# Optimization experiments

Hardware: AMD Instinct MI355X
Metric: run time of the kernel (lower is better)

Reference implementation:

```python
import jax, jax.numpy as jnp
import numpy as np

B, T, D, H = 2, 2048, 1024, 16
HD = D // H  # 64
EPS = 1e-5

def _ln(x, g, b):
    mu = jnp.mean(x, axis=-1, keepdims=True)
    var = jnp.mean(jnp.square(x - mu), axis=-1, keepdims=True)
    return (x - mu) * jax.lax.rsqrt(var + EPS) * g + b

def setup_inputs() -> dict:
    key = jax.random.key(0)
    ks = jax.random.split(key, 12)
    s = 0.02
    return {
        "x":  jax.random.normal(ks[0], (B, T, D), jnp.float32),
        "Wq": jax.random.normal(ks[1], (H, D, HD), jnp.float32) * s,
        "Wk": jax.random.normal(ks[2], (H, D, HD), jnp.float32) * s,
        "Wv": jax.random.normal(ks[3], (H, D, HD), jnp.float32) * s,
        "Wo": jax.random.normal(ks[4], (D, D), jnp.float32) * s,
        "bo": jnp.zeros((D,), jnp.float32),
        "W1": jax.random.normal(ks[5], (D, 4 * D), jnp.float32) * s,
        "b1": jnp.zeros((4 * D,), jnp.float32),
        "W2": jax.random.normal(ks[6], (4 * D, D), jnp.float32) * s,
        "b2": jnp.zeros((D,), jnp.float32),
        "ln1_g": jnp.ones((D,), jnp.float32),
        "ln1_b": jnp.zeros((D,), jnp.float32),
        "ln2_g": jnp.ones((D,), jnp.float32),
        "ln2_b": jnp.zeros((D,), jnp.float32),
    }

def reference(x, Wq, Wk, Wv, Wo, bo, W1, b1, W2, b2, ln1_g, ln1_b, ln2_g, ln2_b):
    b, t, d = x.shape
    # --- self-attention on ln1(x) ---
    h = _ln(x, ln1_g, ln1_b)
    q = jnp.einsum('btd,hde->bhte', h, Wq)  # [B,H,T,hd]
    k = jnp.einsum('btd,hde->bhte', h, Wk)
    v = jnp.einsum('btd,hde->bhte', h, Wv)
    # NOTE: original code scales by C**-0.5 with C = N_EMBED (not head_size)
    wei = jnp.einsum('bhte,bhse->bhts', q, k) * (d ** -0.5)
    causal = jnp.tril(jnp.ones((t, t), bool))
    wei = jnp.where(causal, wei, -jnp.inf)
    att = jax.nn.softmax(wei, axis=-1)
    o = jnp.einsum('bhts,bhse->bhte', att, v)
    o = o.transpose(0, 2, 1, 3).reshape(b, t, d)  # concat heads
    x = x + o @ Wo + bo
    # --- feed-forward on ln2(x) ---
    h2 = _ln(x, ln2_g, ln2_b)
    ff = jax.nn.relu(h2 @ W1 + b1) @ W2 + b2
    return x + ff
```

## Files before the change

### kernel.cpp

```cpp
#include <hip/hip_runtime.h>
#include <stdint.h>

typedef unsigned short u16;
typedef __attribute__((ext_vector_type(8))) short bf16x8;
typedef __attribute__((ext_vector_type(4))) float f32x4;
typedef __attribute__((ext_vector_type(4))) unsigned int u32x4;
typedef __attribute__((ext_vector_type(2))) unsigned int u32x2;
typedef __attribute__((ext_vector_type(4))) unsigned short u16x4;

#define MFMA16(a, b, c) __builtin_amdgcn_mfma_f32_16x16x32_bf16(a, b, c, 0, 0, 0)
#define VMCNT(N) asm volatile("s_waitcnt vmcnt(" #N ")" ::: "memory")
#define LGKM0() asm volatile("s_waitcnt lgkmcnt(0)" ::: "memory")

__device__ __forceinline__ u16 f2bf(float f) {
  union { float f; uint32_t u; } v; v.f = f;
  uint32_t r = v.u + 0x7FFFu + ((v.u >> 16) & 1u);
  return (u16)(r >> 16);
}

__device__ __forceinline__ float bf2f(u16 u) {
  union { uint32_t u; float f; } v; v.u = ((uint32_t)u) << 16;
  return v.f;
}

__device__ __forceinline__ uint32_t cvt_pk_bf16(float a, float b) {
  uint32_t r;
  asm("v_cvt_pk_bf16_f32 %0, %1, %2" : "=v"(r) : "v"(a), "v"(b));
  return r;
}

__device__ __forceinline__ void gload_lds16(const u16* g, u16* l) {
  __builtin_amdgcn_global_load_lds((const __attribute__((address_space(1))) void*)(g),
                                   (__attribute__((address_space(3))) void*)(l), 16, 0, 0);
}

__global__ __launch_bounds__(256) void prep_kernel(
    const float* __restrict__ x, const float* __restrict__ g1,
    const float* __restrict__ be1, u16* __restrict__ h,
    const float* __restrict__ Wq, const float* __restrict__ Wk,
    const float* __restrict__ Wv, u16* __restrict__ BtQKV,
    const float* __restrict__ Wo, u16* __restrict__ WoT,
    const float* __restrict__ W1, u16* __restrict__ W1T,
    const float* __restrict__ W2, u16* __restrict__ W2T) {
  __shared__ float tile[32][33];
  __shared__ float red[8];
  int bid = blockIdx.x, tid = threadIdx.x;
  if (bid < 4096) {
    int row = bid;
    float4 v = ((const float4*)(x + (size_t)row * 1024))[tid];
    float s = v.x + v.y + v.z + v.w;
    float ss = v.x * v.x + v.y * v.y + v.z * v.z + v.w * v.w;
#pragma unroll
    for (int m = 1; m < 64; m <<= 1) { s += __shfl_xor(s, m); ss += __shfl_xor(ss, m); }
    int wave = tid >> 6, lane = tid & 63;
    if (lane == 0) { red[wave] = s; red[4 + wave] = ss; }
    __syncthreads();
    s = red[0] + red[1] + red[2] + red[3];
    ss = red[4] + red[5] + red[6] + red[7];
    float mean = s * (1.0f / 1024.0f);
    float var = ss * (1.0f / 1024.0f) - mean * mean;
    float rstd = rsqrtf(var + 1e-5f);
    float4 gv = ((const float4*)g1)[tid];
    float4 bv = ((const float4*)be1)[tid];
    u16x4 o;
    o.x = f2bf((v.x - mean) * rstd * gv.x + bv.x);
    o.y = f2bf((v.y - mean) * rstd * gv.y + bv.y);
    o.z = f2bf((v.z - mean) * rstd * gv.z + bv.z);
    o.w = f2bf((v.w - mean) * rstd * gv.w + bv.w);
    *(u16x4*)(h + (size_t)row * 1024 + tid * 4) = o;
    return;
  }
  const float* I;
  u16* O;
  int K, N, n0, k0;
  if (bid < 7168) {
    int idx = bid - 4096;
    int bz = idx >> 6, by = (idx >> 1) & 31, bx = idx & 1;
    int ww = bz >> 4, head = bz & 15;
    I = ((ww == 0) ? Wq : (ww == 1) ? Wk : Wv) + (size_t)head * 65536;
    O = BtQKV + (size_t)ww * 1048576 + (size_t)head * 65536;
    K = 1024; N = 64; n0 = bx * 32; k0 = by * 32;
  } else if (bid < 8192) {
    int idx = bid - 7168;
    I = Wo; O = WoT; K = 1024; N = 1024;
    n0 = (idx & 31) * 32; k0 = (idx >> 5) * 32;
  } else if (bid < 12288) {
    int idx = bid - 8192;
    I = W1; O = W1T; K = 1024; N = 4096;
    n0 = (idx & 127) * 32; k0 = (idx >> 7) * 32;
  } else {
    int idx = bid - 12288;
    I = W2; O = W2T; K = 4096; N = 1024;
    n0 = (idx & 31) * 32; k0 = (idx >> 5) * 32;
  }
  int tx = tid & 31, ty = tid >> 5;
#pragma unroll
  for (int i = 0; i < 4; i++)
    tile[ty + i * 8][tx] = I[(size_t)(k0 + ty + i * 8) * N + n0 + tx];
  __syncthreads();
#pragma unroll
  for (int i = 0; i < 4; i++)
    O[(size_t)(n0 + ty + i * 8) * K + k0 + tx] = f2bf(tile[tx][ty + i * 8]);
}

__global__ __launch_bounds__(256) void combine_ln(const float* __restrict__ x,
                                                  const u16* __restrict__ p,
                                                  const float* __restrict__ bo,
                                                  const float* __restrict__ g,
                                                  const float* __restrict__ beta,
                                                  float* __restrict__ out,
                                                  u16* __restrict__ h2) {
  int row = blockIdx.x;
  int tid = threadIdx.x;
  size_t i = (size_t)row * 1024 + tid * 4;
  float4 v = *(const float4*)(x + i);
  float4 bb = *(const float4*)(bo + tid * 4);
  v.x += bb.x; v.y += bb.y; v.z += bb.z; v.w += bb.w;
#pragma unroll
  for (int z = 0; z < 4; z++) {
    u16x4 pv = *(const u16x4*)(p + (size_t)z * 4096 * 1024 + i);
    v.x += bf2f(pv.x); v.y += bf2f(pv.y); v.z += bf2f(pv.z); v.w += bf2f(pv.w);
  }
  *(float4*)(out + i) = v;
  float s = v.x + v.y + v.z + v.w;
  float ss = v.x * v.x + v.y * v.y + v.z * v.z + v.w * v.w;
#pragma unroll
  for (int m = 1; m < 64; m <<= 1) { s += __shfl_xor(s, m); ss += __shfl_xor(ss, m); }
  __shared__ float red[8];
  int wave = tid >> 6, lane = tid & 63;
  if (lane == 0) { red[wave] = s; red[4 + wave] = ss; }
  __syncthreads();
  s = red[0] + red[1] + red[2] + red[3];
  ss = red[4] + red[5] + red[6] + red[7];
  float mean = s * (1.0f / 1024.0f);
  float var = ss * (1.0f / 1024.0f) - mean * mean;
  float rstd = rsqrtf(var + 1e-5f);
  float4 gv = ((const float4*)g)[tid];
  float4 bv = ((const float4*)beta)[tid];
  u16x4 o;
  o.x = f2bf((v.x - mean) * rstd * gv.x + bv.x);
  o.y = f2bf((v.y - mean) * rstd * gv.y + bv.y);
  o.z = f2bf((v.z - mean) * rstd * gv.z + bv.z);
  o.w = f2bf((v.w - mean) * rstd * gv.w + bv.w);
  *(u16x4*)(h2 + i) = o;
}

template <int EP>
__global__ __launch_bounds__(512, 2) void gemm8p(const u16* __restrict__ A,
                                                 const u16* __restrict__ Bt,
                                                 int M, int N, int K, int KS,
                                                 void* __restrict__ out0,
                                                 u16* __restrict__ out1,
                                                 u16* __restrict__ out2,
                                                 const float* __restrict__ bias) {
  __shared__ __align__(16) u16 lds[65536];
  const int tid = threadIdx.x;
  const int lane = tid & 63, wave = tid >> 6;
  const int lo = lane & 15, hi = lane >> 4;
  const int wm = wave >> 2, wn = wave & 3;
  int gx = gridDim.x;
  int lin = blockIdx.y * gx + blockIdx.x;
  int nwg = gx * gridDim.y;
  int cpx = nwg >> 3;
  int swz = (lin & 7) * cpx + (lin >> 3);
  int bm0 = (swz / gx) * 256, bn0 = (swz % gx) * 256;
  int kbeg = blockIdx.z * KS;
  int T = KS >> 6;

  int rs_ = tid >> 3, ss_ = (tid & 7) ^ (rs_ & 7);
  const u16* srcA = A + (size_t)(bm0 + rs_) * K + kbeg + ss_ * 8;
  const u16* srcB = Bt + (size_t)(bn0 + rs_) * K + kbeg + ss_ * 8;
  const size_t i1 = (size_t)64 * K;
  const size_t h1 = (size_t)128 * K;
  const int dst0 = wave * 512;
  const int dst1 = 4096 + wave * 512;

  const int rpA = wm * 16 + lo;
  const int rpB = wn * 16 + lo;
  const int sp0 = (hi ^ (lo & 7)) * 8;

  f32x4 acc[8][4] = {};
  bf16x8 a[4][2], b0[2][2], b1[2][2];

  auto stageA = [&](int buf, int h, int koff) {
    const u16* s = srcA + koff + (h ? h1 : 0);
    u16* d = lds + (buf * 2 + h) * 8192;
    gload_lds16(s, d + dst0);
    gload_lds16(s + i1, d + dst1);
  };
  auto stageB = [&](int buf, int h, int koff) {
    const u16* s = srcB + koff + (h ? h1 : 0);
    u16* d = lds + 32768 + (buf * 2 + h) * 8192;
    gload_lds16(s, d + dst0);
    gload_lds16(s + i1, d + dst1);
  };
  auto loadA = [&](int buf, int h) {
    const u16* base = lds + (buf * 2 + h) * 8192 + rpA * 64;
#pragma unroll
    for (int m = 0; m < 4; m++) {
      a[m][0] = *(const bf16x8*)(base + m * 2048 + sp0);
      a[m][1] = *(const bf16x8*)(base + m * 2048 + (sp0 ^ 32));
    }
  };
  auto loadB = [&](bf16x8 (&bb)[2][2], int buf, int g) {
    const u16* base = lds + 32768 + (buf * 2 + g) * 8192 + rpB * 64;
#pragma unroll
    for (int n = 0; n < 2; n++) {
      bb[n][0] = *(const bf16x8*)(base + n * 4096 + sp0);
      bb[n][1] = *(const bf16x8*)(base + n * 4096 + (sp0 ^ 32));
    }
  };
  auto mmac = [&](int mh, int np, bf16x8 (&bb)[2][2]) {
    __builtin_amdgcn_s_setprio(1);
#pragma unroll
    for (int m = 0; m < 4; m++)
#pragma unroll
      for (int n = 0; n < 2; n++) {
        acc[mh + m][np + n] = MFMA16(a[m][0], bb[n][0], acc[mh + m][np + n]);
        acc[mh + m][np + n] = MFMA16(a[m][1], bb[n][1], acc[mh + m][np + n]);
      }
    __builtin_amdgcn_s_setprio(0);
  };

  stageA(0, 0, 0); stageB(0, 0, 0); stageB(0, 1, 0); stageA(0, 1, 0);
  VMCNT(4);
  __builtin_amdgcn_s_barrier();

  for (int t = 0; t < T; ++t) {
    int cur = t & 1, nxt = cur ^ 1;
    bool more = (t + 1 < T);
    int koff = (t + 1) * 64;
    loadA(cur, 0); loadB(b0, cur, 0);
    if (more) stageA(nxt, 0, koff);
    __builtin_amdgcn_s_barrier();
    LGKM0();
    __builtin_amdgcn_sched_barrier(0);
    mmac(0, 0, b0);
    __builtin_amdgcn_s_barrier();
    loadB(b1, cur, 1);
    if (more) { stageB(nxt, 0, koff); VMCNT(6); } else { VMCNT(2); }
    __builtin_amdgcn_s_barrier();
    LGKM0();
    __builtin_amdgcn_sched_barrier(0);
    mmac(0, 2, b1);
    __builtin_amdgcn_s_barrier();
    loadA(cur, 1);
    if (more) { stageB(nxt, 1, koff); VMCNT(6); } else { VMCNT(0); }
    __builtin_amdgcn_s_barrier();
    LGKM0();
    __builtin_amdgcn_sched_barrier(0);
    mmac(4, 0, b0);
    __builtin_amdgcn_s_barrier();
    if (more) { stageA(nxt, 1, koff); VMCNT(4); }
    __builtin_amdgcn_s_barrier();
    mmac(4, 2, b1);
    __builtin_amdgcn_s_barrier();
  }

  const int sec = (EP == 0) ? (bn0 >> 10) : 0;
#pragma unroll
  for (int mt = 0; mt < 8; mt++) {
    int gr0 = bm0 + (mt >> 2) * 128 + (mt & 3) * 32 + wm * 16 + hi * 4;
#pragma unroll
    for (int nt = 0; nt < 4; nt++) {
      int gc = bn0 + (nt >> 1) * 128 + (nt & 1) * 64 + wn * 16 + lo;
      if constexpr (EP == 0) {
        int b_ = gr0 >> 11, t_ = gr0 & 2047;
        int nn = gc & 1023, h_ = nn >> 6, e_ = nn & 63;
        size_t bh = (size_t)(b_ * 16 + h_);
        if (sec == 2) {
          u32x2 w;
          w.x = cvt_pk_bf16(acc[mt][nt][0], acc[mt][nt][1]);
          w.y = cvt_pk_bf16(acc[mt][nt][2], acc[mt][nt][3]);
          *(u32x2*)(out2 + (bh * 64 + e_) * 2048 + t_) = w;
        } else {
          float sc = (sec == 0) ? 0.0450842200f : 1.0f;
          u16* dst = (sec == 0) ? (u16*)out0 : out1;
#pragma unroll
          for (int j = 0; j < 4; j++)
            dst[(bh * 2048 + t_ + j) * 64 + e_] = f2bf(acc[mt][nt][j] * sc);
        }
      } else {
#pragma unroll
        for (int j = 0; j < 4; j++) {
          int gr = gr0 + j;
          float val = acc[mt][nt][j];
          if constexpr (EP == 2) {
            float v = val + bias[gc];
            ((u16*)out0)[(size_t)gr * N + gc] = f2bf(fmaxf(v, 0.0f));
          } else if constexpr (EP == 4) {
            ((u16*)out0)[(size_t)blockIdx.z * M * N + (size_t)gr * N + gc] = f2bf(val);
          }
        }
      }
    }
  }
}

__global__ __launch_bounds__(256) void combine4(float* __restrict__ out,
                                                const float* __restrict__ res,
                                                const u16* __restrict__ p,
                                                const float* __restrict__ bias) {
  size_t i = ((size_t)blockIdx.x * 256 + threadIdx.x) * 4;
  float4 r = *(const float4*)(res + i);
  float4 bb = *(const float4*)(bias + (i & 1023));
  float a0 = r.x + bb.x, a1 = r.y + bb.y, a2 = r.z + bb.z, a3 = r.w + bb.w;
#pragma unroll
  for (int z = 0; z < 4; z++) {
    u16x4 v = *(const u16x4*)(p + (size_t)z * 4096 * 1024 + i);
    a0 += bf2f(v.x); a1 += bf2f(v.y); a2 += bf2f(v.z); a3 += bf2f(v.w);
  }
  float4 o4 = {a0, a1, a2, a3};
  *(float4*)(out + i) = o4;
}

__global__ __launch_bounds__(512, 4) void attn_kernel(const u16* __restrict__ q,
                                                      const u16* __restrict__ k,
                                                      const u16* __restrict__ vt,
                                                      u16* __restrict__ o) {
  __shared__ __align__(16) u16 Ks[2][64 * 64];
  __shared__ __align__(16) u16 Vs[2][64 * 64];
  __shared__ __align__(16) u16 Ps[8][16 * 72];
  int bh = blockIdx.y;
  int pi = blockIdx.x;
  int tid = threadIdx.x, lane = tid & 63, wave = tid >> 6;
  int lo = lane & 15, hi = lane >> 4;
  int grp = wave >> 2;
  int qblk_w = grp ? pi : (31 - pi);
  int qb0 = qblk_w * 64;
  int nkb = 32 - pi;
  const u16* qbase = q + (size_t)bh * 2048 * 64;
  const u16* kbase = k + (size_t)bh * 2048 * 64;
  const u16* vbase = vt + (size_t)bh * 64 * 2048;

  int srow = tid >> 3;
  int ssl = (tid & 7) ^ (srow & 7);
  int kOff = srow * 64 + ssl * 8;
  int vOff = srow * 2048 + ssl * 8;

  int qrow = qb0 + (wave & 3) * 16 + lo;
  bf16x8 qf0 = *(const bf16x8*)(qbase + (size_t)qrow * 64 + hi * 8);
  bf16x8 qf1 = *(const bf16x8*)(qbase + (size_t)qrow * 64 + 32 + hi * 8);

  float l_r = 0.0f;
  f32x4 of[4] = {};
  u16* Pw = Ps[wave];

  auto stage = [&](int b, int kb) {
    gload_lds16(kbase + (size_t)kb * 4096 + kOff, Ks[b] + wave * 512);
    gload_lds16(vbase + kb * 64 + vOff, Vs[b] + wave * 512);
  };

  stage(0, 0);
  __syncthreads();

  for (int kb = 0; kb < nkb; kb++) {
    int cur = kb & 1;
    if (kb + 1 < nkb) stage(cur ^ 1, kb + 1);
    if (kb <= qblk_w) {
      const u16* Kb = Ks[cur];
      const u16* Vb = Vs[cur];
      f32x4 s4[4] = {};
#pragma unroll
      for (int nt = 0; nt < 4; nt++) {
        int r = nt * 16 + lo, rw = r & 7;
        bf16x8 kf0 = *(const bf16x8*)(Kb + r * 64 + ((hi ^ rw) << 3));
        bf16x8 kf1 = *(const bf16x8*)(Kb + r * 64 + (((hi + 4) ^ rw) << 3));
        s4[nt] = MFMA16(kf0, qf0, s4[nt]);
        s4[nt] = MFMA16(kf1, qf1, s4[nt]);
      }
      float rs = 0.0f;
      bool diag = (kb == qblk_w);
#pragma unroll
      for (int nt = 0; nt < 4; nt++) {
        float e0, e1, e2, e3;
        if (diag) {
          int key = kb * 64 + nt * 16 + hi * 4;
          e0 = (key     > qrow) ? 0.0f : __builtin_amdgcn_exp2f(s4[nt][0]);
          e1 = (key + 1 > qrow) ? 0.0f : __builtin_amdgcn_exp2f(s4[nt][1]);
          e2 = (key + 2 > qrow) ? 0.0f : __builtin_amdgcn_exp2f(s4[nt][2]);
          e3 = (key + 3 > qrow) ? 0.0f : __builtin_amdgcn_exp2f(s4[nt][3]);
        } else {
          e0 = __builtin_amdgcn_exp2f(s4[nt][0]);
          e1 = __builtin_amdgcn_exp2f(s4[nt][1]);
          e2 = __builtin_amdgcn_exp2f(s4[nt][2]);
          e3 = __builtin_amdgcn_exp2f(s4[nt][3]);
        }
        rs += (e0 + e1) + (e2 + e3);
        u32x2 w;
        w.x = cvt_pk_bf16(e0, e1);
        w.y = cvt_pk_bf16(e2, e3);
        *(u32x2*)(Pw + lo * 72 + nt * 16 + hi * 4) = w;
      }
      rs += __shfl_xor(rs, 16);
      rs += __shfl_xor(rs, 32);
      l_r += rs;
      bf16x8 pb0 = *(const bf16x8*)(Pw + lo * 72 + hi * 8);
      bf16x8 pb1 = *(const bf16x8*)(Pw + lo * 72 + 32 + hi * 8);
#pragma unroll
      for (int et = 0; et < 4; et++) {
        int e = et * 16 + lo, ew = e & 7;
        bf16x8 v0 = *(const bf16x8*)(Vb + e * 64 + ((hi ^ ew) << 3));
        bf16x8 v1 = *(const bf16x8*)(Vb + e * 64 + (((hi + 4) ^ ew) << 3));
        of[et] = MFMA16(v0, pb0, of[et]);
        of[et] = MFMA16(v1, pb1, of[et]);
      }
    }
    __syncthreads();
  }
  int hh = bh & 15, bb = bh >> 4;
  float inv = 1.0f / l_r;
  size_t obase = ((size_t)(bb * 2048 + qrow)) * 1024 + hh * 64 + hi * 4;
#pragma unroll
  for (int et = 0; et < 4; et++) {
    u32x2 w;
    w.x = cvt_pk_bf16(of[et][0] * inv, of[et][1] * inv);
    w.y = cvt_pk_bf16(of[et][2] * inv, of[et][3] * inv);
    *(u32x2*)(o + obase + et * 16) = w;
  }
}

extern "C" void kernel_launch(void* const* d_in, const int* in_sizes, int n_in,
                              void* d_out, int out_size, void* d_ws, size_t ws_size,
                              hipStream_t stream) {
  const float* x = (const float*)d_in[0];
  const float* Wq = (const float*)d_in[1];
  const float* Wk = (const float*)d_in[2];
  const float* Wv = (const float*)d_in[3];
  const float* Wo = (const float*)d_in[4];
  const float* bo = (const float*)d_in[5];
  const float* W1 = (const float*)d_in[6];
  const float* b1 = (const float*)d_in[7];
  const float* W2 = (const float*)d_in[8];
  const float* b2 = (const float*)d_in[9];
  const float* g1 = (const float*)d_in[10];
  const float* be1 = (const float*)d_in[11];
  const float* g2 = (const float*)d_in[12];
  const float* be2 = (const float*)d_in[13];
  float* out = (float*)d_out;
  char* ws = (char*)d_ws;
  const size_t MB = 1024ull * 1024ull;

  u16* h = (u16*)(ws + 0);
  u16* o = h;
  u16* BtQKV = (u16*)(ws + 8 * MB);
  u16* WoT = (u16*)(ws + 14 * MB);
  u16* W1T = (u16*)(ws + 16 * MB);
  u16* W2T = (u16*)(ws + 64 * MB);
  u16* qb = (u16*)(ws + 32 * MB);
  u16* kb = (u16*)(ws + 40 * MB);
  u16* vtb = (u16*)(ws + 48 * MB);
  u16* h2 = (u16*)(ws + 8 * MB);
  u16* pwo = (u16*)(ws + 32 * MB);
  u16* yb = (u16*)(ws + 32 * MB);
  u16* pf2 = (u16*)(ws + 0);

  prep_kernel<<<16384, 256, 0, stream>>>(x, g1, be1, h, Wq, Wk, Wv, BtQKV,
                                         Wo, WoT, W1, W1T, W2, W2T);
  gemm8p<0><<<dim3(12, 16), 512, 0, stream>>>(h, BtQKV, 4096, 3072, 1024, 1024,
                                              (void*)qb, kb, vtb, nullptr);
  attn_kernel<<<dim3(16, 32), 512, 0, stream>>>(qb, kb, vtb, o);
  gemm8p<4><<<dim3(4, 16, 4), 512, 0, stream>>>(o, WoT, 4096, 1024, 1024, 256,
                                                (void*)pwo, nullptr, nullptr, nullptr);
  combine_ln<<<4096, 256, 0, stream>>>(x, pwo, bo, g2, be2, out, h2);
  gemm8p<2><<<dim3(16, 16), 512, 0, stream>>>(h2, W1T, 4096, 4096, 1024, 1024,
                                              (void*)yb, nullptr, nullptr, b1);
  gemm8p<4><<<dim3(4, 16, 4), 512, 0, stream>>>(yb, W2T, 4096, 1024, 4096, 1024,
                                                (void*)pf2, nullptr, nullptr, nullptr);
  combine4<<<4096, 256, 0, stream>>>(out, out, pf2, b2);
}
```

Before: 209.5 us.

## Replace split-K output GEMMs with 128x128 tile GEMM fusing bias and residual

The Wo and W2 projections were split-K GEMMs that wrote four bf16 partial outputs, followed by separate combine kernels. They are replaced by a new 128x128-tile GEMM with 256 threads that covers the full K range and adds bias and residual directly in its epilogue, writing fp32. The LN2 kernel now only normalizes. This removes the partial-sum memory traffic and two reduction passes. In exchange there is less parallelism per GEMM (256 workgroups, no K split), and partial sums are no longer rounded to bf16.

```diff
diff --git a/kernel.cpp b/kernel.cpp
--- a/kernel.cpp
+++ b/kernel.cpp
@@ -103,25 +103,13 @@
     O[(size_t)(n0 + ty + i * 8) * K + k0 + tx] = f2bf(tile[tx][ty + i * 8]);
 }
 
-__global__ __launch_bounds__(256) void combine_ln(const float* __restrict__ x,
-                                                  const u16* __restrict__ p,
-                                                  const float* __restrict__ bo,
-                                                  const float* __restrict__ g,
-                                                  const float* __restrict__ beta,
-                                                  float* __restrict__ out,
-                                                  u16* __restrict__ h2) {
+__global__ __launch_bounds__(256) void ln_kernel(const float* __restrict__ x,
+                                                 const float* __restrict__ g,
+                                                 const float* __restrict__ beta,
+                                                 u16* __restrict__ out) {
   int row = blockIdx.x;
   int tid = threadIdx.x;
-  size_t i = (size_t)row * 1024 + tid * 4;
-  float4 v = *(const float4*)(x + i);
-  float4 bb = *(const float4*)(bo + tid * 4);
-  v.x += bb.x; v.y += bb.y; v.z += bb.z; v.w += bb.w;
-#pragma unroll
-  for (int z = 0; z < 4; z++) {
-    u16x4 pv = *(const u16x4*)(p + (size_t)z * 4096 * 1024 + i);
-    v.x += bf2f(pv.x); v.y += bf2f(pv.y); v.z += bf2f(pv.z); v.w += bf2f(pv.w);
-  }
-  *(float4*)(out + i) = v;
+  float4 v = ((const float4*)(x + (size_t)row * 1024))[tid];
   float s = v.x + v.y + v.z + v.w;
   float ss = v.x * v.x + v.y * v.y + v.z * v.z + v.w * v.w;
 #pragma unroll
@@ -142,7 +130,7 @@
   o.y = f2bf((v.y - mean) * rstd * gv.y + bv.y);
   o.z = f2bf((v.z - mean) * rstd * gv.z + bv.z);
   o.w = f2bf((v.w - mean) * rstd * gv.w + bv.w);
-  *(u16x4*)(h2 + i) = o;
+  *(u16x4*)(out + (size_t)row * 1024 + tid * 4) = o;
 }
 
 template <int EP>
@@ -280,38 +268,141 @@
           for (int j = 0; j < 4; j++)
             dst[(bh * 2048 + t_ + j) * 64 + e_] = f2bf(acc[mt][nt][j] * sc);
         }
-      } else {
+      } else if constexpr (EP == 2) {
 #pragma unroll
         for (int j = 0; j < 4; j++) {
           int gr = gr0 + j;
-          float val = acc[mt][nt][j];
-          if constexpr (EP == 2) {
-            float v = val + bias[gc];
-            ((u16*)out0)[(size_t)gr * N + gc] = f2bf(fmaxf(v, 0.0f));
-          } else if constexpr (EP == 4) {
-            ((u16*)out0)[(size_t)blockIdx.z * M * N + (size_t)gr * N + gc] = f2bf(val);
-          }
+          float v = acc[mt][nt][j] + bias[gc];
+          ((u16*)out0)[(size_t)gr * N + gc] = f2bf(fmaxf(v, 0.0f));
         }
       }
     }
   }
 }
 
-__global__ __launch_bounds__(256) void combine4(float* __restrict__ out,
-                                                const float* __restrict__ res,
-                                                const u16* __restrict__ p,
-                                                const float* __restrict__ bias) {
-  size_t i = ((size_t)blockIdx.x * 256 + threadIdx.x) * 4;
-  float4 r = *(const float4*)(res + i);
-  float4 bb = *(const float4*)(bias + (i & 1023));
-  float a0 = r.x + bb.x, a1 = r.y + bb.y, a2 = r.z + bb.z, a3 = r.w + bb.w;
-#pragma unroll
-  for (int z = 0; z < 4; z++) {
-    u16x4 v = *(const u16x4*)(p + (size_t)z * 4096 * 1024 + i);
-    a0 += bf2f(v.x); a1 += bf2f(v.y); a2 += bf2f(v.z); a3 += bf2f(v.w);
-  }
-  float4 o4 = {a0, a1, a2, a3};
-  *(float4*)(out + i) = o4;
+__global__ __launch_bounds__(256, 2) void gemm128(const u16* __restrict__ A,
+                                                  const u16* __restrict__ Bt,
+                                                  int M, int N, int K,
+                                                  const float* __restrict__ bias,
+                                                  const float* __restrict__ res,
+                                                  float* __restrict__ out) {
+  __shared__ __align__(16) u16 lds[32768];
+  const int tid = threadIdx.x;
+  const int lane = tid & 63, wave = tid >> 6;
+  const int lo = lane & 15, hi = lane >> 4;
+  const int wm = wave >> 1, wn = wave & 1;
+  int gx = gridDim.x;
+  int lin = blockIdx.y * gx + blockIdx.x;
+  int nwg = gx * gridDim.y;
+  int cpx = nwg >> 3;
+  int swz = (lin & 7) * cpx + (lin >> 3);
+  int bm0 = (swz / gx) * 128, bn0 = (swz % gx) * 128;
+  int T = K >> 6;
+
+  int rs_ = tid >> 3, ss_ = (tid & 7) ^ (rs_ & 7);
+  const u16* srcA = A + (size_t)(bm0 + rs_) * K + ss_ * 8;
+  const u16* srcB = Bt + (size_t)(bn0 + rs_) * K + ss_ * 8;
+  const size_t i1 = (size_t)32 * K;
+  const size_t h1 = (size_t)64 * K;
+  const int dst0 = wave * 512;
+  const int dst1 = 2048 + wave * 512;
+
+  const int sp0 = (hi ^ (lo & 7)) * 8;
+
+  f32x4 acc[4][4] = {};
+  bf16x8 a[4][2], b[4][2];
+
+  auto stageA = [&](int buf, int h, int koff) {
+    const u16* s = srcA + koff + (h ? h1 : 0);
+    u16* d = lds + (buf * 2 + h) * 4096;
+    gload_lds16(s, d + dst0);
+    gload_lds16(s + i1, d + dst1);
+  };
+  auto stageB = [&](int buf, int h, int koff) {
+    const u16* s = srcB + koff + (h ? h1 : 0);
+    u16* d = lds + 16384 + (buf * 2 + h) * 4096;
+    gload_lds16(s, d + dst0);
+    gload_lds16(s + i1, d + dst1);
+  };
+  auto loadAh = [&](int buf, int h) {
+    const u16* base = lds + (buf * 2 + h) * 4096;
+#pragma unroll
+    for (int m = 0; m < 2; m++) {
+      int lr = m * 32 + wm * 16 + lo;
+      a[h * 2 + m][0] = *(const bf16x8*)(base + lr * 64 + sp0);
+      a[h * 2 + m][1] = *(const bf16x8*)(base + lr * 64 + (sp0 ^ 32));
+    }
+  };
+  auto loadBh = [&](int buf, int h) {
+    const u16* base = lds + 16384 + (buf * 2 + h) * 4096;
+#pragma unroll
+    for (int n = 0; n < 2; n++) {
+      int lr = n * 32 + wn * 16 + lo;
+      b[h * 2 + n][0] = *(const bf16x8*)(base + lr * 64 + sp0);
+      b[h * 2 + n][1] = *(const bf16x8*)(base + lr * 64 + (sp0 ^ 32));
+    }
+  };
+  auto mmac = [&](int mb, int nb) {
+    __builtin_amdgcn_s_setprio(1);
+#pragma unroll
+    for (int m = 0; m < 2; m++)
+#pragma unroll
+      for (int n = 0; n < 2; n++) {
+        acc[mb + m][nb + n] = MFMA16(a[mb + m][0], b[nb + n][0], acc[mb + m][nb + n]);
+        acc[mb + m][nb + n] = MFMA16(a[mb + m][1], b[nb + n][1], acc[mb + m][nb + n]);
+      }
+    __builtin_amdgcn_s_setprio(0);
+  };
+
+  stageA(0, 0, 0); stageB(0, 0, 0); stageB(0, 1, 0); stageA(0, 1, 0);
+  VMCNT(4);
+  __builtin_amdgcn_s_barrier();
+
+  for (int t = 0; t < T; ++t) {
+    int cur = t & 1, nxt = cur ^ 1;
+    bool more = (t + 1 < T);
+    int koff = (t + 1) * 64;
+    loadAh(cur, 0); loadBh(cur, 0);
+    if (more) { stageA(nxt, 0, koff); VMCNT(4); } else { VMCNT(2); }
+    __builtin_amdgcn_s_barrier();
+    LGKM0();
+    __builtin_amdgcn_sched_barrier(0);
+    mmac(0, 0);
+    __builtin_amdgcn_s_barrier();
+    loadBh(cur, 1);
+    if (more) { stageB(nxt, 0, koff); VMCNT(4); } else { VMCNT(0); }
+    __builtin_amdgcn_s_barrier();
+    LGKM0();
+    __builtin_amdgcn_sched_barrier(0);
+    mmac(0, 2);
+    __builtin_amdgcn_s_barrier();
+    loadAh(cur, 1);
+    if (more) stageB(nxt, 1, koff);
+    __builtin_amdgcn_s_barrier();
+    LGKM0();
+    __builtin_amdgcn_sched_barrier(0);
+    mmac(2, 0);
+    __builtin_amdgcn_s_barrier();
+    if (more) { stageA(nxt, 1, koff); VMCNT(4); }
+    __builtin_amdgcn_s_barrier();
+    mmac(2, 2);
+    __builtin_amdgcn_s_barrier();
+  }
+
+#pragma unroll
+  for (int mt = 0; mt < 4; mt++) {
+    int gr0 = bm0 + mt * 32 + wm * 16 + hi * 4;
+#pragma unroll
+    for (int nt = 0; nt < 4; nt++) {
+      int gc = bn0 + nt * 32 + wn * 16 + lo;
+      float bb = bias[gc];
+#pragma unroll
+      for (int j = 0; j < 4; j++) {
+        int gr = gr0 + j;
+        out[(size_t)gr * N + gc] = acc[mt][nt][j] + bb + res[(size_t)gr * N + gc];
+      }
+    }
+  }
 }
 
 __global__ __launch_bounds__(512, 4) void attn_kernel(const u16* __restrict__ q,
@@ -451,21 +542,16 @@
   u16* kb = (u16*)(ws + 40 * MB);
   u16* vtb = (u16*)(ws + 48 * MB);
   u16* h2 = (u16*)(ws + 8 * MB);
-  u16* pwo = (u16*)(ws + 32 * MB);
   u16* yb = (u16*)(ws + 32 * MB);
-  u16* pf2 = (u16*)(ws + 0);
 
   prep_kernel<<<16384, 256, 0, stream>>>(x, g1, be1, h, Wq, Wk, Wv, BtQKV,
                                          Wo, WoT, W1, W1T, W2, W2T);
   gemm8p<0><<<dim3(12, 16), 512, 0, stream>>>(h, BtQKV, 4096, 3072, 1024, 1024,
                                               (void*)qb, kb, vtb, nullptr);
   attn_kernel<<<dim3(16, 32), 512, 0, stream>>>(qb, kb, vtb, o);
-  gemm8p<4><<<dim3(4, 16, 4), 512, 0, stream>>>(o, WoT, 4096, 1024, 1024, 256,
-                                                (void*)pwo, nullptr, nullptr, nullptr);
-  combine_ln<<<4096, 256, 0, stream>>>(x, pwo, bo, g2, be2, out, h2);
+  gemm128<<<dim3(8, 32), 256, 0, stream>>>(o, WoT, 4096, 1024, 1024, bo, x, out);
+  ln_kernel<<<4096, 256, 0, stream>>>(out, g2, be2, h2);
   gemm8p<2><<<dim3(16, 16), 512, 0, stream>>>(h2, W1T, 4096, 4096, 1024, 1024,
                                               (void*)yb, nullptr, nullptr, b1);
-  gemm8p<4><<<dim3(4, 16, 4), 512, 0, stream>>>(yb, W2T, 4096, 1024, 4096, 1024,
-                                                (void*)pf2, nullptr, nullptr, nullptr);
-  combine4<<<4096, 256, 0, stream>>>(out, out, pf2, b2);
-}
+  gemm128<<<dim3(8, 32), 256, 0, stream>>>(yb, W2T, 4096, 1024, 4096, b2, out, out);
+}
```

Measured after the change: 207.8 us. Within noise of the previous version (-0.8%).
